# Kernel optimization log

Hardware: AMD Instinct MI355X
Metric: run time of the kernel (lower is better)

Reference implementation:

```python
import jax, jax.numpy as jnp
import numpy as np

MARGIN = 0.3

def setup_inputs() -> dict:
    key = jax.random.key(0)
    k1, k2 = jax.random.split(key)
    embeddings = jax.random.normal(k1, (8192, 512), dtype=jnp.float32)
    labels = jax.random.randint(k2, (8192,), 0, 128, dtype=jnp.int64)
    return {"embeddings": embeddings, "labels": labels}

def _pairwise_euclidean(x):
    # ||xi - xj|| via GEMM, matching torch reference (relu clamp + sqrt(.+1e-16))
    dot = x @ x.T                      # [B, B]
    sq = jnp.diagonal(dot)             # [B]
    d2 = sq[None, :] - 2.0 * dot + sq[:, None]
    d2 = jnp.maximum(d2, 0.0)
    return jnp.sqrt(d2 + 1e-16)

def reference(embeddings, labels):
    n = embeddings.shape[0]
    d = _pairwise_euclidean(embeddings)                 # [B, B]
    same = labels[:, None] == labels[None, :]           # [B, B]
    eye = jnp.eye(n, dtype=bool)
    mask_pos = same & ~eye
    mask_neg = ~same
    # fused masked row-wise reductions (hard mining)
    hardest_pos = jnp.max(jnp.where(mask_pos, d, -jnp.inf), axis=1)  # [B]
    hardest_neg = jnp.min(jnp.where(mask_neg, d, jnp.inf), axis=1)   # [B]
    valid = mask_pos.any(axis=1) & mask_neg.any(axis=1)              # [B]
    per_row = jax.nn.relu(hardest_pos - hardest_neg + MARGIN)
    per_row = jnp.where(valid, per_row, 0.0)
    denom = jnp.maximum(jnp.sum(valid.astype(per_row.dtype)), 1.0)
    return jnp.sum(per_row) / denom
```

## Files before the change

kernel.cpp:

```cpp
#include <hip/hip_runtime.h>

#define BATCH 8192
#define DIM   512
#define NTILE 1152

typedef __attribute__((ext_vector_type(4))) float  f32x4;
typedef __attribute__((ext_vector_type(8))) __bf16 bf16x8;

__device__ __forceinline__ unsigned short f2bf(float x) {
  unsigned u = __float_as_uint(x);
  u = (u + 0x7FFFu + ((u >> 16) & 1u)) >> 16;
  return (unsigned short)u;
}

__device__ __forceinline__ void load_lds16(const void* g, void* l) {
  __builtin_amdgcn_global_load_lds(
      (__attribute__((address_space(1))) void*)(g),
      (__attribute__((address_space(3))) void*)(l), 16, 0, 0);
}

__device__ __forceinline__ unsigned enc(float f) {
  unsigned u = __float_as_uint(f);
  return u ^ (unsigned)(((int)u >> 31) | 0x80000000);
}
__device__ __forceinline__ float dec(unsigned k) {
  unsigned u = (k & 0x80000000u) ? (k ^ 0x80000000u) : ~k;
  return __uint_as_float(u);
}

__global__ __launch_bounds__(256) void prep_kernel(
    const float* __restrict__ X, unsigned short* __restrict__ Xb,
    float* __restrict__ sq, unsigned* __restrict__ ctrl,
    uint4* __restrict__ pos4, uint4* __restrict__ neg4) {
  int gid = blockIdx.x * 256 + threadIdx.x;
  if (gid == 0) {
    ((float*)ctrl)[0] = 0.f;
    ((float*)ctrl)[1] = 0.f;
    ctrl[2] = 0u;
    ctrl[3] = 0u;
  }
  if (gid < 196608) {
    pos4[gid] = (uint4){0u, 0u, 0u, 0u};
    neg4[gid] = (uint4){~0u, ~0u, ~0u, ~0u};
  }
  int wave = threadIdx.x >> 6, lane = threadIdx.x & 63;
  int row = blockIdx.x * 4 + wave;
  const float4* xr = (const float4*)(X + (size_t)row * DIM);
  float4 a = xr[lane * 2];
  float4 b = xr[lane * 2 + 1];
  float s = a.x*a.x + a.y*a.y + a.z*a.z + a.w*a.w
          + b.x*b.x + b.y*b.y + b.z*b.z + b.w*b.w;
  uint4 p;
  p.x = (unsigned)f2bf(a.x) | ((unsigned)f2bf(a.y) << 16);
  p.y = (unsigned)f2bf(a.z) | ((unsigned)f2bf(a.w) << 16);
  p.z = (unsigned)f2bf(b.x) | ((unsigned)f2bf(b.y) << 16);
  p.w = (unsigned)f2bf(b.z) | ((unsigned)f2bf(b.w) << 16);
  ((uint4*)(Xb + (size_t)row * DIM))[lane] = p;
  #pragma unroll
  for (int off = 32; off > 0; off >>= 1) s += __shfl_down(s, off);
  if (lane == 0) sq[row] = s;
}

template<int NI>
__device__ __forceinline__ void gemm_tile(
    const unsigned short* __restrict__ Xb, int i0, int jw,
    unsigned short* Asm, unsigned short* Bsm,
    int wave, int wm, int wn, int quad, int lc, int rc, int gcol,
    f32x4 (&acc)[4][8]) {
  for (int k0 = 0; k0 < DIM; k0 += 64) {
    #pragma unroll
    for (int tt = 0; tt < 4; tt++) {
      int c = wave * 4 + tt;
      int row = c * 8 + rc;
      load_lds16(Xb + (size_t)(i0 + row) * DIM + k0 + gcol, &Asm[c * 512]);
    }
    #pragma unroll
    for (int tt = 0; tt < NI; tt++) {
      int c = wave * NI + tt;
      int row = c * 8 + rc;
      load_lds16(Xb + (size_t)(jw + row) * DIM + k0 + gcol, &Bsm[c * 512]);
    }
    __syncthreads();
    #pragma unroll
    for (int kk = 0; kk < 64; kk += 32) {
      int kc = kk >> 3;
      int asel = ((kc + quad) ^ (lc & 7)) * 8;
      bf16x8 af[4], bfr[NI];
      #pragma unroll
      for (int mi = 0; mi < 4; mi++)
        af[mi] = *(const bf16x8*)&Asm[(wm * 64 + mi * 16 + lc) * 64 + asel];
      #pragma unroll
      for (int ni = 0; ni < NI; ni++)
        bfr[ni] = *(const bf16x8*)&Bsm[(wn * (NI * 16) + ni * 16 + lc) * 64 + asel];
      #pragma unroll
      for (int mi = 0; mi < 4; mi++)
        #pragma unroll
        for (int ni = 0; ni < NI; ni++)
          acc[mi][ni] = __builtin_amdgcn_mfma_f32_16x16x32_bf16(
              af[mi], bfr[ni], acc[mi][ni], 0, 0, 0);
    }
    __syncthreads();
  }
}

template<bool STRAD, int NI, int WNS>
__device__ __forceinline__ void epilogue(
    const f32x4 (&acc)[4][8], const float* __restrict__ sq,
    const int* __restrict__ labels,
    int i0, int jwin, int wm, int wn, int quad, int lc,
    unsigned (*ibuf)[128][2], unsigned (*jbuf)[256][2]) {
  float sqj_r[NI]; int labj_r[NI];
  #pragma unroll
  for (int ni = 0; ni < NI; ni++) {
    int j = jwin + wn * WNS + ni * 16 + lc;
    sqj_r[ni] = sq[j]; labj_r[ni] = labels[j];
  }
  float rpos[16], rneg[16];
  float jp[NI], jn[NI];
  #pragma unroll
  for (int x = 0; x < NI; x++) { jp[x] = -3e38f; jn[x] = 3e38f; }
  #pragma unroll
  for (int mi = 0; mi < 4; mi++) {
    #pragma unroll
    for (int r = 0; r < 4; r++) {
      int ig = i0 + wm * 64 + mi * 16 + quad * 4 + r;
      int li = labels[ig];
      float si = sq[ig];
      float rp = -3e38f, rn = 3e38f;
      #pragma unroll
      for (int ni = 0; ni < NI; ni++) {
        float a = acc[mi][ni][r];
        float v = fmaf(-2.f, a, sqj_r[ni]);
        bool same = (li == labj_r[ni]);
        bool posok = same;
        if (STRAD) posok = same && ((jwin + wn * WNS + ni * 16 + lc) != ig);
        rp = fmaxf(rp, posok ? v : -3e38f);
        rn = fminf(rn, same ? 3e38f : v);
        if (!STRAD) {
          float v2 = fmaf(-2.f, a, si);
          jp[ni] = fmaxf(jp[ni], same ? v2 : -3e38f);
          jn[ni] = fminf(jn[ni], same ? 3e38f : v2);
        }
      }
      rpos[mi * 4 + r] = rp; rneg[mi * 4 + r] = rn;
    }
  }
  #pragma unroll
  for (int m = 1; m <= 8; m <<= 1)
    #pragma unroll
    for (int x = 0; x < 16; x++) {
      rpos[x] = fmaxf(rpos[x], __shfl_xor(rpos[x], m));
      rneg[x] = fminf(rneg[x], __shfl_xor(rneg[x], m));
    }
  if (lc == 0) {
    #pragma unroll
    for (int mi = 0; mi < 4; mi++)
      #pragma unroll
      for (int r = 0; r < 4; r++) {
        int row = wm * 64 + mi * 16 + quad * 4 + r;
        ibuf[wn][row][0] = enc(rpos[mi * 4 + r]);
        ibuf[wn][row][1] = enc(rneg[mi * 4 + r]);
      }
  }
  if (!STRAD) {
    #pragma unroll
    for (int m = 16; m <= 32; m <<= 1)
      #pragma unroll
      for (int x = 0; x < NI; x++) {
        jp[x] = fmaxf(jp[x], __shfl_xor(jp[x], m));
        jn[x] = fminf(jn[x], __shfl_xor(jn[x], m));
      }
    if (quad == 0) {
      #pragma unroll
      for (int ni = 0; ni < NI; ni++) {
        int col = wn * WNS + ni * 16 + lc;
        jbuf[wm][col][0] = enc(jp[ni]);
        jbuf[wm][col][1] = enc(jn[ni]);
      }
    }
  }
}

__global__ __launch_bounds__(256, 2) void triplet_mfma(
    const unsigned short* __restrict__ Xb, const float* __restrict__ sq,
    const int* __restrict__ labels, unsigned* __restrict__ ctrl,
    unsigned* __restrict__ pos_i, unsigned* __restrict__ neg_i,
    unsigned* __restrict__ pos_j, unsigned* __restrict__ neg_j) {
  __shared__ __align__(16) unsigned short Asm[128 * 64];
  __shared__ __align__(16) unsigned short Bsm[256 * 64];
  __shared__ int tshare;

  unsigned (*ibuf)[128][2] = reinterpret_cast<unsigned (*)[128][2]>(&Asm[0]);
  unsigned (*jbuf)[256][2] = reinterpret_cast<unsigned (*)[256][2]>(&Asm[1024]);

  int tid = threadIdx.x;
  int wave = tid >> 6, lane = tid & 63;
  int wm = wave >> 1, wn = wave & 1;
  int quad = lane >> 4, lc = lane & 15;
  int rc = lane >> 3;
  int gcol = ((lane & 7) ^ rc) * 8;

  for (;;) {
    if (tid == 0) tshare = (int)atomicAdd(&ctrl[3], 1u);
    __syncthreads();
    int t = tshare;
    if (t >= NTILE) break;

    int It = 0, Js = 0, q = -1; bool strad = false;
    if (t < 64) { It = t; Js = t >> 1; strad = true; }
    else {
      int u;
      if (t < 1024) u = t - 64;
      else { q = (t - 1024) & 3; u = 960 + ((t - 1024) >> 2); }
      for (int s = 0; s < 64; s++) {
        int c = 31 - (s >> 1);
        if (u < c) { It = s; Js = (s >> 1) + 1 + u; break; }
        u -= c;
      }
    }
    int i0 = It * 128;
    int jw = Js * 256 + (q >= 0 ? q * 64 : 0);

    f32x4 acc[4][8];
    #pragma unroll
    for (int mi = 0; mi < 4; mi++)
      #pragma unroll
      for (int ni = 0; ni < 8; ni++)
        acc[mi][ni] = (f32x4){0.f, 0.f, 0.f, 0.f};

    if (q >= 0) {
      gemm_tile<2>(Xb, i0, jw, Asm, Bsm, wave, wm, wn, quad, lc, rc, gcol, acc);
      epilogue<false, 2, 32>(acc, sq, labels, i0, jw, wm, wn, quad, lc, ibuf, jbuf);
    } else {
      gemm_tile<8>(Xb, i0, jw, Asm, Bsm, wave, wm, wn, quad, lc, rc, gcol, acc);
      if (strad)
        epilogue<true, 8, 128>(acc, sq, labels, i0, jw, wm, wn, quad, lc, ibuf, jbuf);
      else
        epilogue<false, 8, 128>(acc, sq, labels, i0, jw, wm, wn, quad, lc, ibuf, jbuf);
    }
    __syncthreads();

    if (q >= 0) {
      if (tid < 128) {
        unsigned p = max(ibuf[0][tid][0], ibuf[1][tid][0]);
        unsigned n = min(ibuf[0][tid][1], ibuf[1][tid][1]);
        atomicMax(&pos_i[(size_t)Js * BATCH + i0 + tid], p);
        atomicMin(&neg_i[(size_t)Js * BATCH + i0 + tid], n);
      }
      if (tid < 64) {
        unsigned p = max(jbuf[0][tid][0], jbuf[1][tid][0]);
        unsigned n = min(jbuf[0][tid][1], jbuf[1][tid][1]);
        pos_j[(size_t)It * BATCH + jw + tid] = p;
        neg_j[(size_t)It * BATCH + jw + tid] = n;
      }
    } else {
      if (tid < 128) {
        unsigned p = max(ibuf[0][tid][0], ibuf[1][tid][0]);
        unsigned n = min(ibuf[0][tid][1], ibuf[1][tid][1]);
        pos_i[(size_t)Js * BATCH + i0 + tid] = p;
        neg_i[(size_t)Js * BATCH + i0 + tid] = n;
      }
      if (!strad) {
        unsigned p = max(jbuf[0][tid][0], jbuf[1][tid][0]);
        unsigned n = min(jbuf[0][tid][1], jbuf[1][tid][1]);
        pos_j[(size_t)It * BATCH + jw + tid] = p;
        neg_j[(size_t)It * BATCH + jw + tid] = n;
      }
    }
    __syncthreads();
  }
}

__global__ __launch_bounds__(256) void final_kernel(
    const unsigned* __restrict__ pos_i, const unsigned* __restrict__ neg_i,
    const unsigned* __restrict__ pos_j, const unsigned* __restrict__ neg_j,
    const float* __restrict__ sq, unsigned* __restrict__ ctrl,
    float* __restrict__ out) {
  int i = blockIdx.x * 256 + threadIdx.x;
  unsigned pe = 0u, ne = 0xFFFFFFFFu;
  #pragma unroll 4
  for (int s = 0; s < 32; s++) {
    pe = max(pe, pos_i[(size_t)s * BATCH + i]);
    ne = min(ne, neg_i[(size_t)s * BATCH + i]);
  }
  #pragma unroll 4
  for (int s = 0; s < 64; s++) {
    pe = max(pe, pos_j[(size_t)s * BATCH + i]);
    ne = min(ne, neg_j[(size_t)s * BATCH + i]);
  }
  float p = dec(pe), n = dec(ne);
  float term = 0.f, cnt = 0.f;
  if (p > -1e37f && n < 1e37f) {
    float si = sq[i];
    float dp = sqrtf(fmaxf(si + p, 0.f) + 1e-16f);
    float dn = sqrtf(fmaxf(si + n, 0.f) + 1e-16f);
    term = fmaxf(dp - dn + 0.3f, 0.f);
    cnt = 1.f;
  }
  #pragma unroll
  for (int off = 32; off > 0; off >>= 1) {
    term += __shfl_down(term, off);
    cnt  += __shfl_down(cnt, off);
  }
  __shared__ float ss[4], sc[4];
  int wave = threadIdx.x >> 6, lane = threadIdx.x & 63;
  if (lane == 0) { ss[wave] = term; sc[wave] = cnt; }
  __syncthreads();
  if (threadIdx.x == 0) {
    atomicAdd((float*)&ctrl[0], ss[0] + ss[1] + ss[2] + ss[3]);
    atomicAdd((float*)&ctrl[1], sc[0] + sc[1] + sc[2] + sc[3]);
    __threadfence();
    unsigned t = atomicAdd(&ctrl[2], 1u);
    if (t == 31u) {
      float S = atomicAdd((float*)&ctrl[0], 0.f);
      float C = atomicAdd((float*)&ctrl[1], 0.f);
      out[0] = S / fmaxf(C, 1.f);
    }
  }
}

extern "C" void kernel_launch(void* const* d_in, const int* in_sizes, int n_in,
                              void* d_out, int out_size, void* d_ws, size_t ws_size,
                              hipStream_t stream) {
  const float* X      = (const float*)d_in[0];
  const int*   labels = (const int*)d_in[1];
  float* out = (float*)d_out;
  char* ws = (char*)d_ws;

  const size_t SLOT = (size_t)BATCH * 4;
  unsigned short* Xb = (unsigned short*)ws;
  float* sq      = (float*)(ws + (8u << 20));
  unsigned* ctrl = (unsigned*)(ws + (8u << 20) + (32u << 10));
  char*  posb = ws + (8u << 20) + (64u << 10);
  char*  negb = posb + 96 * SLOT;
  unsigned* pos_i = (unsigned*)posb;
  unsigned* pos_j = (unsigned*)(posb + 32 * SLOT);
  unsigned* neg_i = (unsigned*)negb;
  unsigned* neg_j = (unsigned*)(negb + 32 * SLOT);

  prep_kernel<<<BATCH / 4, 256, 0, stream>>>(X, Xb, sq, ctrl,
                                             (uint4*)posb, (uint4*)negb);
  triplet_mfma<<<512, 256, 0, stream>>>(Xb, sq, labels, ctrl,
                                        pos_i, neg_i, pos_j, neg_j);
  final_kernel<<<BATCH / 256, 256, 0, stream>>>(pos_i, neg_i, pos_j, neg_j, sq, ctrl, out);
}
```

Measured before the change: 135.4 us.

## Triple-buffer GEMM K-loop with async LDS loads and vmcnt waits

Replaces the single-buffer K-loop (load 64-wide K slab, sync, compute, sync) with a 3-stage ring of 32-wide K slabs. Global-to-LDS loads for two future stages stay in flight while the current one is computed, using explicit s_waitcnt vmcnt counts and bare s_barrier instead of __syncthreads. The aim is to hide global load latency behind MFMA work. LDS use grows from 48KB to 72KB, which may limit occupancy to fewer than 2 blocks per CU, and the swizzle is changed to fit the 32-wide layout.

```diff
diff --git a/kernel.cpp b/kernel.cpp
--- a/kernel.cpp
+++ b/kernel.cpp
@@ -17,6 +17,19 @@
   __builtin_amdgcn_global_load_lds(
       (__attribute__((address_space(1))) void*)(g),
       (__attribute__((address_space(3))) void*)(l), 16, 0, 0);
+}
+
+template<int N> __device__ __forceinline__ void waitcnt_vm() {
+  if constexpr (N == 12)     asm volatile("s_waitcnt vmcnt(12)" ::: "memory");
+  else if constexpr (N == 6) asm volatile("s_waitcnt vmcnt(6)"  ::: "memory");
+  else if constexpr (N == 3) asm volatile("s_waitcnt vmcnt(3)"  ::: "memory");
+  else                       asm volatile("s_waitcnt vmcnt(0)"  ::: "memory");
+}
+
+__device__ __forceinline__ void barrier_nofence() {
+  asm volatile("" ::: "memory");
+  __builtin_amdgcn_s_barrier();
+  asm volatile("" ::: "memory");
 }
 
 __device__ __forceinline__ unsigned enc(float f) {
@@ -62,44 +75,61 @@
 }
 
 template<int NI>
+__device__ __forceinline__ void stage(
+    const unsigned short* __restrict__ Xb, int i0, int jw, int k,
+    unsigned short* buf, int wave, int lane) {
+  int r4 = lane >> 2;
+  int sc = (lane & 3) ^ (r4 & 3);
+  int koff = k + sc * 8;
+  #pragma unroll
+  for (int tt = 0; tt < 2; tt++) {
+    int c = wave * 2 + tt;
+    load_lds16(Xb + (size_t)(i0 + c * 16 + r4) * DIM + koff, buf + c * 512);
+  }
+  constexpr int NB = NI / 2;
+  #pragma unroll
+  for (int tt = 0; tt < NB; tt++) {
+    int c = wave * NB + tt;
+    load_lds16(Xb + (size_t)(jw + c * 16 + r4) * DIM + koff, buf + 4096 + c * 512);
+  }
+}
+
+template<int NI>
 __device__ __forceinline__ void gemm_tile(
     const unsigned short* __restrict__ Xb, int i0, int jw,
-    unsigned short* Asm, unsigned short* Bsm,
-    int wave, int wm, int wn, int quad, int lc, int rc, int gcol,
+    unsigned short* r0, unsigned short* r1, unsigned short* r2,
+    int wave, int wm, int wn, int quad, int lc, int lane,
     f32x4 (&acc)[4][8]) {
-  for (int k0 = 0; k0 < DIM; k0 += 64) {
-    #pragma unroll
-    for (int tt = 0; tt < 4; tt++) {
-      int c = wave * 4 + tt;
-      int row = c * 8 + rc;
-      load_lds16(Xb + (size_t)(i0 + row) * DIM + k0 + gcol, &Asm[c * 512]);
-    }
-    #pragma unroll
-    for (int tt = 0; tt < NI; tt++) {
-      int c = wave * NI + tt;
-      int row = c * 8 + rc;
-      load_lds16(Xb + (size_t)(jw + row) * DIM + k0 + gcol, &Bsm[c * 512]);
-    }
-    __syncthreads();
-    #pragma unroll
-    for (int kk = 0; kk < 64; kk += 32) {
-      int kc = kk >> 3;
-      int asel = ((kc + quad) ^ (lc & 7)) * 8;
-      bf16x8 af[4], bfr[NI];
-      #pragma unroll
-      for (int mi = 0; mi < 4; mi++)
-        af[mi] = *(const bf16x8*)&Asm[(wm * 64 + mi * 16 + lc) * 64 + asel];
+  constexpr int S = 2 + NI / 2;
+  unsigned short *bc = r0, *bn = r1, *bt = r2;
+  stage<NI>(Xb, i0, jw, 0,  bc, wave, lane);
+  stage<NI>(Xb, i0, jw, 32, bn, wave, lane);
+  int aoff = (quad ^ (lc & 3)) * 8;
+  for (int t = 0; t < 16; t++) {
+    if (t < 14) {
+      stage<NI>(Xb, i0, jw, (t + 2) * 32, bt, wave, lane);
+      waitcnt_vm<2 * S>();
+    } else if (t == 14) {
+      waitcnt_vm<S>();
+    } else {
+      waitcnt_vm<0>();
+    }
+    barrier_nofence();
+    bf16x8 af[4], bfr[NI];
+    #pragma unroll
+    for (int mi = 0; mi < 4; mi++)
+      af[mi] = *(const bf16x8*)&bc[(wm * 64 + mi * 16 + lc) * 32 + aoff];
+    #pragma unroll
+    for (int ni = 0; ni < NI; ni++)
+      bfr[ni] = *(const bf16x8*)&bc[4096 + (wn * (NI * 16) + ni * 16 + lc) * 32 + aoff];
+    #pragma unroll
+    for (int mi = 0; mi < 4; mi++)
       #pragma unroll
       for (int ni = 0; ni < NI; ni++)
-        bfr[ni] = *(const bf16x8*)&Bsm[(wn * (NI * 16) + ni * 16 + lc) * 64 + asel];
-      #pragma unroll
-      for (int mi = 0; mi < 4; mi++)
-        #pragma unroll
-        for (int ni = 0; ni < NI; ni++)
-          acc[mi][ni] = __builtin_amdgcn_mfma_f32_16x16x32_bf16(
-              af[mi], bfr[ni], acc[mi][ni], 0, 0, 0);
-    }
-    __syncthreads();
+        acc[mi][ni] = __builtin_amdgcn_mfma_f32_16x16x32_bf16(
+            af[mi], bfr[ni], acc[mi][ni], 0, 0, 0);
+    barrier_nofence();
+    unsigned short* tp = bc; bc = bn; bn = bt; bt = tp;
   }
 }
 
@@ -186,19 +216,16 @@
     const int* __restrict__ labels, unsigned* __restrict__ ctrl,
     unsigned* __restrict__ pos_i, unsigned* __restrict__ neg_i,
     unsigned* __restrict__ pos_j, unsigned* __restrict__ neg_j) {
-  __shared__ __align__(16) unsigned short Asm[128 * 64];
-  __shared__ __align__(16) unsigned short Bsm[256 * 64];
+  __shared__ __align__(16) unsigned short ring[3][12288];
   __shared__ int tshare;
 
-  unsigned (*ibuf)[128][2] = reinterpret_cast<unsigned (*)[128][2]>(&Asm[0]);
-  unsigned (*jbuf)[256][2] = reinterpret_cast<unsigned (*)[256][2]>(&Asm[1024]);
+  unsigned (*ibuf)[128][2] = reinterpret_cast<unsigned (*)[128][2]>(&ring[0][0]);
+  unsigned (*jbuf)[256][2] = reinterpret_cast<unsigned (*)[256][2]>(&ring[0][1024]);
 
   int tid = threadIdx.x;
   int wave = tid >> 6, lane = tid & 63;
   int wm = wave >> 1, wn = wave & 1;
   int quad = lane >> 4, lc = lane & 15;
-  int rc = lane >> 3;
-  int gcol = ((lane & 7) ^ rc) * 8;
 
   for (;;) {
     if (tid == 0) tshare = (int)atomicAdd(&ctrl[3], 1u);
@@ -229,10 +256,12 @@
         acc[mi][ni] = (f32x4){0.f, 0.f, 0.f, 0.f};
 
     if (q >= 0) {
-      gemm_tile<2>(Xb, i0, jw, Asm, Bsm, wave, wm, wn, quad, lc, rc, gcol, acc);
+      gemm_tile<2>(Xb, i0, jw, ring[0], ring[1], ring[2],
+                   wave, wm, wn, quad, lc, lane, acc);
       epilogue<false, 2, 32>(acc, sq, labels, i0, jw, wm, wn, quad, lc, ibuf, jbuf);
     } else {
-      gemm_tile<8>(Xb, i0, jw, Asm, Bsm, wave, wm, wn, quad, lc, rc, gcol, acc);
+      gemm_tile<8>(Xb, i0, jw, ring[0], ring[1], ring[2],
+                   wave, wm, wn, quad, lc, lane, acc);
       if (strad)
         epilogue<true, 8, 128>(acc, sq, labels, i0, jw, wm, wn, quad, lc, ibuf, jbuf);
       else
```

Measured after the change: 142.3 us. 5.0% more time.

## Fuse prep, GEMM-mining and final reduction into one persistent kernel

Applied to the files above, without the earlier changes.

Merges the bf16 conversion/row-norm prep, the tiled MFMA hard-mining pass and the final per-row reduction into a single persistent kernel of 512 blocks. The phases are separated by software grid barriers built on atomic counters. The pos/neg partial buffers and control words are now initialised with hipMemsetAsync instead of inside the prep kernel. It also raises wave priority around the MFMA block with s_setprio. This removes two kernel launches and their gaps, but the grid barrier depends on all 512 blocks being co-resident and adds spin-wait time, and three memset calls are added.

```diff
diff --git a/kernel.cpp b/kernel.cpp
--- a/kernel.cpp
+++ b/kernel.cpp
@@ -3,6 +3,7 @@
 #define BATCH 8192
 #define DIM   512
 #define NTILE 1152
+#define NBLK  512
 
 typedef __attribute__((ext_vector_type(4))) float  f32x4;
 typedef __attribute__((ext_vector_type(8))) __bf16 bf16x8;
@@ -26,39 +27,6 @@
 __device__ __forceinline__ float dec(unsigned k) {
   unsigned u = (k & 0x80000000u) ? (k ^ 0x80000000u) : ~k;
   return __uint_as_float(u);
-}
-
-__global__ __launch_bounds__(256) void prep_kernel(
-    const float* __restrict__ X, unsigned short* __restrict__ Xb,
-    float* __restrict__ sq, unsigned* __restrict__ ctrl,
-    uint4* __restrict__ pos4, uint4* __restrict__ neg4) {
-  int gid = blockIdx.x * 256 + threadIdx.x;
-  if (gid == 0) {
-    ((float*)ctrl)[0] = 0.f;
-    ((float*)ctrl)[1] = 0.f;
-    ctrl[2] = 0u;
-    ctrl[3] = 0u;
-  }
-  if (gid < 196608) {
-    pos4[gid] = (uint4){0u, 0u, 0u, 0u};
-    neg4[gid] = (uint4){~0u, ~0u, ~0u, ~0u};
-  }
-  int wave = threadIdx.x >> 6, lane = threadIdx.x & 63;
-  int row = blockIdx.x * 4 + wave;
-  const float4* xr = (const float4*)(X + (size_t)row * DIM);
-  float4 a = xr[lane * 2];
-  float4 b = xr[lane * 2 + 1];
-  float s = a.x*a.x + a.y*a.y + a.z*a.z + a.w*a.w
-          + b.x*b.x + b.y*b.y + b.z*b.z + b.w*b.w;
-  uint4 p;
-  p.x = (unsigned)f2bf(a.x) | ((unsigned)f2bf(a.y) << 16);
-  p.y = (unsigned)f2bf(a.z) | ((unsigned)f2bf(a.w) << 16);
-  p.z = (unsigned)f2bf(b.x) | ((unsigned)f2bf(b.y) << 16);
-  p.w = (unsigned)f2bf(b.z) | ((unsigned)f2bf(b.w) << 16);
-  ((uint4*)(Xb + (size_t)row * DIM))[lane] = p;
-  #pragma unroll
-  for (int off = 32; off > 0; off >>= 1) s += __shfl_down(s, off);
-  if (lane == 0) sq[row] = s;
 }
 
 template<int NI>
@@ -92,12 +60,14 @@
       #pragma unroll
       for (int ni = 0; ni < NI; ni++)
         bfr[ni] = *(const bf16x8*)&Bsm[(wn * (NI * 16) + ni * 16 + lc) * 64 + asel];
+      __builtin_amdgcn_s_setprio(1);
       #pragma unroll
       for (int mi = 0; mi < 4; mi++)
         #pragma unroll
         for (int ni = 0; ni < NI; ni++)
           acc[mi][ni] = __builtin_amdgcn_mfma_f32_16x16x32_bf16(
               af[mi], bfr[ni], acc[mi][ni], 0, 0, 0);
+      __builtin_amdgcn_s_setprio(0);
     }
     __syncthreads();
   }
@@ -181,17 +151,20 @@
   }
 }
 
-__global__ __launch_bounds__(256, 2) void triplet_mfma(
-    const unsigned short* __restrict__ Xb, const float* __restrict__ sq,
-    const int* __restrict__ labels, unsigned* __restrict__ ctrl,
+__global__ __launch_bounds__(256, 2) void triplet_fused(
+    const float* __restrict__ X, const int* __restrict__ labels,
+    unsigned short* __restrict__ Xb, float* __restrict__ sq,
+    unsigned* __restrict__ ctrl,
     unsigned* __restrict__ pos_i, unsigned* __restrict__ neg_i,
-    unsigned* __restrict__ pos_j, unsigned* __restrict__ neg_j) {
+    unsigned* __restrict__ pos_j, unsigned* __restrict__ neg_j,
+    float* __restrict__ out) {
   __shared__ __align__(16) unsigned short Asm[128 * 64];
   __shared__ __align__(16) unsigned short Bsm[256 * 64];
   __shared__ int tshare;
 
   unsigned (*ibuf)[128][2] = reinterpret_cast<unsigned (*)[128][2]>(&Asm[0]);
   unsigned (*jbuf)[256][2] = reinterpret_cast<unsigned (*)[256][2]>(&Asm[1024]);
+  unsigned (*fbuf)[16][2]  = reinterpret_cast<unsigned (*)[16][2]>(&Asm[3072]);
 
   int tid = threadIdx.x;
   int wave = tid >> 6, lane = tid & 63;
@@ -199,6 +172,34 @@
   int quad = lane >> 4, lc = lane & 15;
   int rc = lane >> 3;
   int gcol = ((lane & 7) ^ rc) * 8;
+
+  #pragma unroll
+  for (int it = 0; it < 4; it++) {
+    int row = blockIdx.x * 16 + it * 4 + wave;
+    const float4* xr = (const float4*)(X + (size_t)row * DIM);
+    float4 a = xr[lane * 2];
+    float4 b = xr[lane * 2 + 1];
+    float s = a.x*a.x + a.y*a.y + a.z*a.z + a.w*a.w
+            + b.x*b.x + b.y*b.y + b.z*b.z + b.w*b.w;
+    uint4 p;
+    p.x = (unsigned)f2bf(a.x) | ((unsigned)f2bf(a.y) << 16);
+    p.y = (unsigned)f2bf(a.z) | ((unsigned)f2bf(a.w) << 16);
+    p.z = (unsigned)f2bf(b.x) | ((unsigned)f2bf(b.y) << 16);
+    p.w = (unsigned)f2bf(b.z) | ((unsigned)f2bf(b.w) << 16);
+    ((uint4*)(Xb + (size_t)row * DIM))[lane] = p;
+    #pragma unroll
+    for (int off = 32; off > 0; off >>= 1) s += __shfl_down(s, off);
+    if (lane == 0) sq[row] = s;
+  }
+
+  __threadfence();
+  __syncthreads();
+  if (tid == 0) {
+    atomicAdd(&ctrl[4], 1u);
+    while (atomicAdd(&ctrl[4], 0u) < NBLK) __builtin_amdgcn_s_sleep(8);
+  }
+  __syncthreads();
+  __threadfence();
 
   for (;;) {
     if (tid == 0) tshare = (int)atomicAdd(&ctrl[3], 1u);
@@ -269,52 +270,64 @@
     }
     __syncthreads();
   }
-}
-
-__global__ __launch_bounds__(256) void final_kernel(
-    const unsigned* __restrict__ pos_i, const unsigned* __restrict__ neg_i,
-    const unsigned* __restrict__ pos_j, const unsigned* __restrict__ neg_j,
-    const float* __restrict__ sq, unsigned* __restrict__ ctrl,
-    float* __restrict__ out) {
-  int i = blockIdx.x * 256 + threadIdx.x;
-  unsigned pe = 0u, ne = 0xFFFFFFFFu;
-  #pragma unroll 4
-  for (int s = 0; s < 32; s++) {
-    pe = max(pe, pos_i[(size_t)s * BATCH + i]);
-    ne = min(ne, neg_i[(size_t)s * BATCH + i]);
-  }
-  #pragma unroll 4
-  for (int s = 0; s < 64; s++) {
-    pe = max(pe, pos_j[(size_t)s * BATCH + i]);
-    ne = min(ne, neg_j[(size_t)s * BATCH + i]);
-  }
-  float p = dec(pe), n = dec(ne);
-  float term = 0.f, cnt = 0.f;
-  if (p > -1e37f && n < 1e37f) {
-    float si = sq[i];
-    float dp = sqrtf(fmaxf(si + p, 0.f) + 1e-16f);
-    float dn = sqrtf(fmaxf(si + n, 0.f) + 1e-16f);
-    term = fmaxf(dp - dn + 0.3f, 0.f);
-    cnt = 1.f;
-  }
-  #pragma unroll
-  for (int off = 32; off > 0; off >>= 1) {
-    term += __shfl_down(term, off);
-    cnt  += __shfl_down(cnt, off);
-  }
-  __shared__ float ss[4], sc[4];
-  int wave = threadIdx.x >> 6, lane = threadIdx.x & 63;
-  if (lane == 0) { ss[wave] = term; sc[wave] = cnt; }
+
+  __threadfence();
   __syncthreads();
-  if (threadIdx.x == 0) {
-    atomicAdd((float*)&ctrl[0], ss[0] + ss[1] + ss[2] + ss[3]);
-    atomicAdd((float*)&ctrl[1], sc[0] + sc[1] + sc[2] + sc[3]);
-    __threadfence();
-    unsigned t = atomicAdd(&ctrl[2], 1u);
-    if (t == 31u) {
-      float S = atomicAdd((float*)&ctrl[0], 0.f);
-      float C = atomicAdd((float*)&ctrl[1], 0.f);
-      out[0] = S / fmaxf(C, 1.f);
+  if (tid == 0) {
+    atomicAdd(&ctrl[5], 1u);
+    while (atomicAdd(&ctrl[5], 0u) < NBLK) __builtin_amdgcn_s_sleep(8);
+  }
+  __syncthreads();
+  __threadfence();
+
+  {
+    int i = blockIdx.x * 16 + lc;
+    int g = wave * 4 + quad;
+    unsigned pe = 0u, ne = 0xFFFFFFFFu;
+    #pragma unroll
+    for (int s = 0; s < 32; s += 16) {
+      pe = max(pe, pos_i[(size_t)(g + s) * BATCH + i]);
+      ne = min(ne, neg_i[(size_t)(g + s) * BATCH + i]);
+    }
+    #pragma unroll
+    for (int s = 0; s < 64; s += 16) {
+      pe = max(pe, pos_j[(size_t)(g + s) * BATCH + i]);
+      ne = min(ne, neg_j[(size_t)(g + s) * BATCH + i]);
+    }
+    pe = max(pe, __shfl_xor(pe, 16)); ne = min(ne, __shfl_xor(ne, 16));
+    pe = max(pe, __shfl_xor(pe, 32)); ne = min(ne, __shfl_xor(ne, 32));
+    if (lane < 16) { fbuf[wave][lane][0] = pe; fbuf[wave][lane][1] = ne; }
+    __syncthreads();
+    if (wave == 0 && lane < 16) {
+      pe = max(max(fbuf[0][lane][0], fbuf[1][lane][0]),
+               max(fbuf[2][lane][0], fbuf[3][lane][0]));
+      ne = min(min(fbuf[0][lane][1], fbuf[1][lane][1]),
+               min(fbuf[2][lane][1], fbuf[3][lane][1]));
+      float p = dec(pe), n = dec(ne);
+      float term = 0.f, cnt = 0.f;
+      if (p > -1e37f && n < 1e37f) {
+        float si = sq[blockIdx.x * 16 + lane];
+        float dp = sqrtf(fmaxf(si + p, 0.f) + 1e-16f);
+        float dn = sqrtf(fmaxf(si + n, 0.f) + 1e-16f);
+        term = fmaxf(dp - dn + 0.3f, 0.f);
+        cnt = 1.f;
+      }
+      #pragma unroll
+      for (int off = 8; off > 0; off >>= 1) {
+        term += __shfl_down(term, off);
+        cnt  += __shfl_down(cnt, off);
+      }
+      if (lane == 0) {
+        atomicAdd((float*)&ctrl[0], term);
+        atomicAdd((float*)&ctrl[1], cnt);
+        __threadfence();
+        unsigned tk = atomicAdd(&ctrl[2], 1u);
+        if (tk == NBLK - 1) {
+          float S = atomicAdd((float*)&ctrl[0], 0.f);
+          float C = atomicAdd((float*)&ctrl[1], 0.f);
+          out[0] = S / fmaxf(C, 1.f);
+        }
+      }
     }
   }
 }
@@ -338,9 +351,9 @@
   unsigned* neg_i = (unsigned*)negb;
   unsigned* neg_j = (unsigned*)(negb + 32 * SLOT);
 
-  prep_kernel<<<BATCH / 4, 256, 0, stream>>>(X, Xb, sq, ctrl,
-                                             (uint4*)posb, (uint4*)negb);
-  triplet_mfma<<<512, 256, 0, stream>>>(Xb, sq, labels, ctrl,
-                                        pos_i, neg_i, pos_j, neg_j);
-  final_kernel<<<BATCH / 256, 256, 0, stream>>>(pos_i, neg_i, pos_j, neg_j, sq, ctrl, out);
-}
+  hipMemsetAsync(ctrl, 0, 64, stream);
+  hipMemsetAsync(posb, 0x00, 96 * SLOT, stream);
+  hipMemsetAsync(negb, 0xFF, 96 * SLOT, stream);
+  triplet_fused<<<NBLK, 256, 0, stream>>>(X, labels, Xb, sq, ctrl,
+                                          pos_i, neg_i, pos_j, neg_j, out);
+}
```

Result: slower. 371.5 us (+174.3%).

## Fuse final reduction into persistent GEMM kernel via grid-wide arrival barrier

Applied to the files above, without the earlier changes.

Removes the separate final_kernel launch. The last 128 blocks to finish the tiled GEMM loop wait on an atomic arrival counter until every block is done, then each reduces 64 rows of the partial pos/neg buffers across four waves and accumulates the loss. This saves one kernel launch and its tail, and spreads the reduction over more blocks. In exchange it relies on all 512 blocks being co-resident for the spin-wait to be safe, and the waiting blocks stay idle while they spin.

```diff
diff --git a/kernel.cpp b/kernel.cpp
--- a/kernel.cpp
+++ b/kernel.cpp
@@ -3,6 +3,8 @@
 #define BATCH 8192
 #define DIM   512
 #define NTILE 1152
+#define NBLK  512
+#define NRED  128
 
 typedef __attribute__((ext_vector_type(4))) float  f32x4;
 typedef __attribute__((ext_vector_type(8))) __bf16 bf16x8;
@@ -38,6 +40,8 @@
     ((float*)ctrl)[1] = 0.f;
     ctrl[2] = 0u;
     ctrl[3] = 0u;
+    ctrl[4] = 0u;
+    ctrl[5] = 0u;
   }
   if (gid < 196608) {
     pos4[gid] = (uint4){0u, 0u, 0u, 0u};
@@ -185,13 +189,16 @@
     const unsigned short* __restrict__ Xb, const float* __restrict__ sq,
     const int* __restrict__ labels, unsigned* __restrict__ ctrl,
     unsigned* __restrict__ pos_i, unsigned* __restrict__ neg_i,
-    unsigned* __restrict__ pos_j, unsigned* __restrict__ neg_j) {
+    unsigned* __restrict__ pos_j, unsigned* __restrict__ neg_j,
+    float* __restrict__ out) {
   __shared__ __align__(16) unsigned short Asm[128 * 64];
   __shared__ __align__(16) unsigned short Bsm[256 * 64];
   __shared__ int tshare;
+  __shared__ unsigned sh_rank;
 
   unsigned (*ibuf)[128][2] = reinterpret_cast<unsigned (*)[128][2]>(&Asm[0]);
   unsigned (*jbuf)[256][2] = reinterpret_cast<unsigned (*)[256][2]>(&Asm[1024]);
+  unsigned (*fbuf)[64][2]  = reinterpret_cast<unsigned (*)[64][2]>(&Asm[3072]);
 
   int tid = threadIdx.x;
   int wave = tid >> 6, lane = tid & 63;
@@ -269,52 +276,70 @@
     }
     __syncthreads();
   }
-}
-
-__global__ __launch_bounds__(256) void final_kernel(
-    const unsigned* __restrict__ pos_i, const unsigned* __restrict__ neg_i,
-    const unsigned* __restrict__ pos_j, const unsigned* __restrict__ neg_j,
-    const float* __restrict__ sq, unsigned* __restrict__ ctrl,
-    float* __restrict__ out) {
-  int i = blockIdx.x * 256 + threadIdx.x;
+
+  __threadfence();
+  __syncthreads();
+  if (tid == 0) sh_rank = atomicAdd(&ctrl[4], 1u);
+  __syncthreads();
+  unsigned rank = sh_rank;
+  if (rank < NBLK - NRED) return;
+
+  if (tid == 0) {
+    unsigned v = __hip_atomic_load(&ctrl[4], __ATOMIC_RELAXED, __HIP_MEMORY_SCOPE_AGENT);
+    while (v < NBLK) {
+      __builtin_amdgcn_s_sleep(16);
+      v = __hip_atomic_load(&ctrl[4], __ATOMIC_RELAXED, __HIP_MEMORY_SCOPE_AGENT);
+    }
+  }
+  __syncthreads();
+  __threadfence();
+
+  int part = (int)rank - (NBLK - NRED);
+  int r = part * 64 + lane;
+  int g = wave;
   unsigned pe = 0u, ne = 0xFFFFFFFFu;
-  #pragma unroll 4
-  for (int s = 0; s < 32; s++) {
-    pe = max(pe, pos_i[(size_t)s * BATCH + i]);
-    ne = min(ne, neg_i[(size_t)s * BATCH + i]);
-  }
-  #pragma unroll 4
-  for (int s = 0; s < 64; s++) {
-    pe = max(pe, pos_j[(size_t)s * BATCH + i]);
-    ne = min(ne, neg_j[(size_t)s * BATCH + i]);
-  }
-  float p = dec(pe), n = dec(ne);
-  float term = 0.f, cnt = 0.f;
-  if (p > -1e37f && n < 1e37f) {
-    float si = sq[i];
-    float dp = sqrtf(fmaxf(si + p, 0.f) + 1e-16f);
-    float dn = sqrtf(fmaxf(si + n, 0.f) + 1e-16f);
-    term = fmaxf(dp - dn + 0.3f, 0.f);
-    cnt = 1.f;
-  }
-  #pragma unroll
-  for (int off = 32; off > 0; off >>= 1) {
-    term += __shfl_down(term, off);
-    cnt  += __shfl_down(cnt, off);
-  }
-  __shared__ float ss[4], sc[4];
-  int wave = threadIdx.x >> 6, lane = threadIdx.x & 63;
-  if (lane == 0) { ss[wave] = term; sc[wave] = cnt; }
+  #pragma unroll
+  for (int k = 0; k < 24; k++) {
+    int s = g * 24 + k;
+    const unsigned* ps = (s < 32) ? pos_i + (size_t)s * BATCH
+                                  : pos_j + (size_t)(s - 32) * BATCH;
+    const unsigned* ns = (s < 32) ? neg_i + (size_t)s * BATCH
+                                  : neg_j + (size_t)(s - 32) * BATCH;
+    pe = max(pe, ps[r]);
+    ne = min(ne, ns[r]);
+  }
+  fbuf[wave][lane][0] = pe;
+  fbuf[wave][lane][1] = ne;
   __syncthreads();
-  if (threadIdx.x == 0) {
-    atomicAdd((float*)&ctrl[0], ss[0] + ss[1] + ss[2] + ss[3]);
-    atomicAdd((float*)&ctrl[1], sc[0] + sc[1] + sc[2] + sc[3]);
-    __threadfence();
-    unsigned t = atomicAdd(&ctrl[2], 1u);
-    if (t == 31u) {
-      float S = atomicAdd((float*)&ctrl[0], 0.f);
-      float C = atomicAdd((float*)&ctrl[1], 0.f);
-      out[0] = S / fmaxf(C, 1.f);
+  if (wave == 0) {
+    pe = max(max(fbuf[0][lane][0], fbuf[1][lane][0]),
+             max(fbuf[2][lane][0], fbuf[3][lane][0]));
+    ne = min(min(fbuf[0][lane][1], fbuf[1][lane][1]),
+             min(fbuf[2][lane][1], fbuf[3][lane][1]));
+    float p = dec(pe), n = dec(ne);
+    float term = 0.f, cnt = 0.f;
+    if (p > -1e37f && n < 1e37f) {
+      float si = sq[part * 64 + lane];
+      float dp = sqrtf(fmaxf(si + p, 0.f) + 1e-16f);
+      float dn = sqrtf(fmaxf(si + n, 0.f) + 1e-16f);
+      term = fmaxf(dp - dn + 0.3f, 0.f);
+      cnt = 1.f;
+    }
+    #pragma unroll
+    for (int off = 32; off > 0; off >>= 1) {
+      term += __shfl_down(term, off);
+      cnt  += __shfl_down(cnt, off);
+    }
+    if (lane == 0) {
+      atomicAdd((float*)&ctrl[0], term);
+      atomicAdd((float*)&ctrl[1], cnt);
+      __threadfence();
+      unsigned tk = atomicAdd(&ctrl[2], 1u);
+      if (tk == NRED - 1) {
+        float S = atomicAdd((float*)&ctrl[0], 0.f);
+        float C = atomicAdd((float*)&ctrl[1], 0.f);
+        out[0] = S / fmaxf(C, 1.f);
+      }
     }
   }
 }
@@ -340,7 +365,6 @@
 
   prep_kernel<<<BATCH / 4, 256, 0, stream>>>(X, Xb, sq, ctrl,
                                              (uint4*)posb, (uint4*)negb);
-  triplet_mfma<<<512, 256, 0, stream>>>(Xb, sq, labels, ctrl,
-                                        pos_i, neg_i, pos_j, neg_j);
-  final_kernel<<<BATCH / 256, 256, 0, stream>>>(pos_i, neg_i, pos_j, neg_j, sq, ctrl, out);
-}
+  triplet_mfma<<<NBLK, 256, 0, stream>>>(Xb, sq, labels, ctrl,
+                                         pos_i, neg_i, pos_j, neg_j, out);
+}
```

Result: slower. 179.0 us (+32.1%).
